# Kernel optimization log

Hardware: AMD Instinct MI355X
Metric: run time of the kernel (lower is better)

The kernel has to match this reference:

```python
import jax, jax.numpy as jnp
from jax import lax
import numpy as np

T, B, I, H, O = 256, 128, 1024, 1024, 512
SIGMA = 0.05

def setup_inputs() -> dict:
    key = jax.random.key(0)
    ks = jax.random.split(key, 16)
    x = jax.random.normal(ks[0], (T, B, I), dtype=jnp.float32)
    r_noise = jax.random.uniform(ks[1], (T, B, I), dtype=jnp.float32) * SIGMA
    z_noise = jax.random.uniform(ks[2], (T, B, I), dtype=jnp.float32) * SIGMA
    h_noise = jax.random.uniform(ks[3], (T, B, I), dtype=jnp.float32) * SIGMA
    si = 1.0 / np.sqrt(I)
    sh = 1.0 / np.sqrt(H)
    Wxz = jax.random.normal(ks[4], (H, I), dtype=jnp.float32) * si
    Wxr = jax.random.normal(ks[5], (H, I), dtype=jnp.float32) * si
    Wxh = jax.random.normal(ks[6], (H, I), dtype=jnp.float32) * si
    Whz = jax.random.normal(ks[7], (H, H), dtype=jnp.float32) * sh
    Whr = jax.random.normal(ks[8], (H, H), dtype=jnp.float32) * sh
    Whh = jax.random.normal(ks[9], (H, H), dtype=jnp.float32) * sh  # rec_scale_factor = 1.0
    bz = jnp.zeros((H,), dtype=jnp.float32)
    br = jnp.zeros((H,), dtype=jnp.float32)
    bh = jnp.zeros((H,), dtype=jnp.float32)
    Wout = jax.random.normal(ks[10], (O, H), dtype=jnp.float32) * sh
    bout = jnp.zeros((O,), dtype=jnp.float32)
    return {"x": x, "r_noise": r_noise, "z_noise": z_noise, "h_noise": h_noise,
            "Wxz": Wxz, "Wxr": Wxr, "Wxh": Wxh, "Whz": Whz, "bz": bz,
            "Whr": Whr, "br": br, "Whh": Whh, "bh": bh, "Wout": Wout, "bout": bout}

def reference(x, r_noise, z_noise, h_noise, Wxz, Wxr, Wxh, Whz, bz, Whr, br, Whh, bh, Wout, bout):
    # x: [T, B, I]; hidden state h: [B, H]
    h0 = jnp.zeros((x.shape[1], Whh.shape[0]), dtype=x.dtype)
    def step(h, inp):
        xt, rn, zn, hn = inp
        R = jax.nn.sigmoid((xt + rn) @ Wxr.T + h @ Whr.T + br)
        Z = jax.nn.sigmoid((xt + zn) @ Wxz.T + h @ Whz.T + bz)
        H_hat = jnp.tanh((xt + hn) @ Wxh.T + (R * h) @ Whh.T + bh)
        h_new = Z * h + (1.0 - Z) * H_hat
        return h_new, h_new
    _, hidden_states = lax.scan(step, h0, (x, r_noise, z_noise, h_noise))  # [T, B, H]
    out = hidden_states @ Wout.T + bout  # [T, B, O]
    return out
```

## Files before the change

### kernel.cpp

```cpp
#include <hip/hip_runtime.h>

typedef _Float16 f16;
typedef _Float16 f16x8 __attribute__((ext_vector_type(8)));
typedef _Float16 f16x4 __attribute__((ext_vector_type(4)));
typedef float    f32x4 __attribute__((ext_vector_type(4)));

#define T_STEPS 256
#define B_ROWS  128
#define I_DIM   1024
#define H_DIM   1024
#define O_DIM   512
#define TBROWS  (T_STEPS * B_ROWS)
#define BH      (B_ROWS * H_DIM)
#define NWG     64

__global__ void k_init(unsigned* flg) {
    for (int i = threadIdx.x; i < (8 * NWG + 8) * 16; i += 256) flg[i] = 0u;
}

template<int K>
__device__ __forceinline__ f16x8 gload(const f16* p) {
    f16x8 r;
    asm volatile("global_load_dwordx4 %0, %1, off offset:%c2"
                 : "=v"(r) : "v"(p), "n"(K * 64));
    return r;
}
template<int K> struct Iss {
    static __device__ __forceinline__ void go(f16x8* fr, const f16* p) {
        fr[K] = gload<K>(p);
        Iss<K + 1>::go(fr, p);
    }
};
template<> struct Iss<32> {
    static __device__ __forceinline__ void go(f16x8*, const f16*) {}
};
__device__ __forceinline__ void gstore8_cc(f16* p, f16x4 v) {
    asm volatile("global_store_dwordx2 %0, %1, off sc0 sc1"
                 :: "v"(p), "v"(v) : "memory");
}

__device__ __forceinline__ void wpub(unsigned* flg, int grp, int wg, unsigned gen, int lane) {
    asm volatile("s_waitcnt vmcnt(0) lgkmcnt(0)" ::: "memory");
    if (lane == 0)
        __hip_atomic_store(&flg[(grp * NWG + wg) * 16], gen, __ATOMIC_RELAXED, __HIP_MEMORY_SCOPE_AGENT);
    __builtin_amdgcn_sched_barrier(0);
}
__device__ __forceinline__ void wpoll(unsigned* flg, unsigned* agg, int grp, int wg, unsigned gen, int lane) {
    if (wg == grp) {
        while (__hip_atomic_load(&flg[(grp * NWG + lane) * 16], __ATOMIC_RELAXED, __HIP_MEMORY_SCOPE_AGENT) < gen)
            __builtin_amdgcn_s_sleep(1);
        if (lane < 2)
            __hip_atomic_store(&agg[grp * 16 + lane], gen, __ATOMIC_RELAXED, __HIP_MEMORY_SCOPE_AGENT);
    } else {
        while (__hip_atomic_load(&agg[grp * 16 + (lane & 1)], __ATOMIC_RELAXED, __HIP_MEMORY_SCOPE_AGENT) < gen)
            __builtin_amdgcn_s_sleep(1);
    }
    __builtin_amdgcn_sched_barrier(0);
}

__global__ __launch_bounds__(256) void k_gate_gemm(
    const float* __restrict__ x,
    const float* __restrict__ nR, const float* __restrict__ nZ, const float* __restrict__ nH,
    const float* __restrict__ WxR, const float* __restrict__ WxZ, const float* __restrict__ WxH,
    f16* __restrict__ GR, f16* __restrict__ GZ, f16* __restrict__ GH)
{
    const int g = blockIdx.z;
    const float* noise = (g == 0) ? nR : (g == 1) ? nZ : nH;
    const float* W     = (g == 0) ? WxR : (g == 1) ? WxZ : WxH;
    f16* G             = (g == 0) ? GR : (g == 1) ? GZ : GH;

    __shared__ f16 As[128 * 40];
    __shared__ f16 Bs[128 * 40];

    const int t = threadIdx.x;
    const int lane = t & 63;
    const int w  = t >> 6;
    const int wm = w & 1, wn = w >> 1;
    const int bid = blockIdx.x;
    const int l   = (bid & 7) * 256 + (bid >> 3);
    const int rowBase = (l >> 3) * 128;
    const int colBase = (l & 7) * 128;

    const int srow = t >> 1;
    const int sk   = (t & 1) * 16;

    f32x4 acc[4][4] = {};

    for (int kt = 0; kt < I_DIM; kt += 32) {
        {
            const float* xp = x     + (size_t)(rowBase + srow) * I_DIM + kt + sk;
            const float* np = noise + (size_t)(rowBase + srow) * I_DIM + kt + sk;
            f16x8 t0, t1;
            #pragma unroll
            for (int q = 0; q < 2; ++q) {
                float4 a = ((const float4*)xp)[q];
                float4 b = ((const float4*)np)[q];
                t0[q*4+0] = (f16)(a.x + b.x); t0[q*4+1] = (f16)(a.y + b.y);
                t0[q*4+2] = (f16)(a.z + b.z); t0[q*4+3] = (f16)(a.w + b.w);
            }
            #pragma unroll
            for (int q = 0; q < 2; ++q) {
                float4 a = ((const float4*)xp)[q+2];
                float4 b = ((const float4*)np)[q+2];
                t1[q*4+0] = (f16)(a.x + b.x); t1[q*4+1] = (f16)(a.y + b.y);
                t1[q*4+2] = (f16)(a.z + b.z); t1[q*4+3] = (f16)(a.w + b.w);
            }
            *(f16x8*)&As[srow*40 + sk]     = t0;
            *(f16x8*)&As[srow*40 + sk + 8] = t1;
            const float* wp = W + (size_t)(colBase + srow) * I_DIM + kt + sk;
            #pragma unroll
            for (int q = 0; q < 2; ++q) {
                float4 a = ((const float4*)wp)[q];
                t0[q*4+0] = (f16)a.x; t0[q*4+1] = (f16)a.y; t0[q*4+2] = (f16)a.z; t0[q*4+3] = (f16)a.w;
            }
            #pragma unroll
            for (int q = 0; q < 2; ++q) {
                float4 a = ((const float4*)wp)[q+2];
                t1[q*4+0] = (f16)a.x; t1[q*4+1] = (f16)a.y; t1[q*4+2] = (f16)a.z; t1[q*4+3] = (f16)a.w;
            }
            *(f16x8*)&Bs[srow*40 + sk]     = t0;
            *(f16x8*)&Bs[srow*40 + sk + 8] = t1;
        }
        __syncthreads();
        f16x8 af[4], bf[4];
        #pragma unroll
        for (int i = 0; i < 4; ++i)
            af[i] = *(const f16x8*)&As[(wm*64 + i*16 + (lane & 15))*40 + ((lane >> 4) * 8)];
        #pragma unroll
        for (int i = 0; i < 4; ++i)
            bf[i] = *(const f16x8*)&Bs[(wn*64 + i*16 + (lane & 15))*40 + ((lane >> 4) * 8)];
        #pragma unroll
        for (int i = 0; i < 4; ++i)
            #pragma unroll
            for (int j = 0; j < 4; ++j)
                acc[i][j] = __builtin_amdgcn_mfma_f32_16x16x32_f16(af[i], bf[j], acc[i][j], 0, 0, 0);
        __syncthreads();
    }
    #pragma unroll
    for (int i = 0; i < 4; ++i) {
        const int row = rowBase + wm*64 + i*16 + ((lane >> 4) * 4);
        #pragma unroll
        for (int j = 0; j < 4; ++j) {
            const int col = colBase + wn*64 + j*16 + (lane & 15);
            #pragma unroll
            for (int r = 0; r < 4; ++r)
                G[(size_t)(row + r) * H_DIM + col] = (f16)acc[i][j][r];
        }
    }
}

__global__ __launch_bounds__(256) void k_out_gemm(
    const f16* __restrict__ Hs, const float* __restrict__ Wout,
    const float* __restrict__ bout, float* __restrict__ out)
{
    __shared__ f16 As[128 * 40];
    __shared__ f16 Bs[128 * 40];

    const int t = threadIdx.x;
    const int lane = t & 63;
    const int w  = t >> 6;
    const int wm = w & 1, wn = w >> 1;
    const int bid = blockIdx.x;
    const int l   = (bid & 7) * 128 + (bid >> 3);
    const int rowBase = (l >> 2) * 128;
    const int colBase = (l & 3) * 128;

    const int srow = t >> 1;
    const int sk   = (t & 1) * 16;

    f32x4 acc[4][4] = {};

    for (int kt = 0; kt < H_DIM; kt += 32) {
        {
            const f16* ap = Hs + (size_t)(rowBase + srow) * H_DIM + kt + sk;
            *(f16x8*)&As[srow*40 + sk]     = *(const f16x8*)ap;
            *(f16x8*)&As[srow*40 + sk + 8] = *(const f16x8*)(ap + 8);
            const float* wp = Wout + (size_t)(colBase + srow) * H_DIM + kt + sk;
            f16x8 t0, t1;
            #pragma unroll
            for (int q = 0; q < 2; ++q) {
                float4 a = ((const float4*)wp)[q];
                t0[q*4+0] = (f16)a.x; t0[q*4+1] = (f16)a.y; t0[q*4+2] = (f16)a.z; t0[q*4+3] = (f16)a.w;
            }
            #pragma unroll
            for (int q = 0; q < 2; ++q) {
                float4 a = ((const float4*)wp)[q+2];
                t1[q*4+0] = (f16)a.x; t1[q*4+1] = (f16)a.y; t1[q*4+2] = (f16)a.z; t1[q*4+3] = (f16)a.w;
            }
            *(f16x8*)&Bs[srow*40 + sk]     = t0;
            *(f16x8*)&Bs[srow*40 + sk + 8] = t1;
        }
        __syncthreads();
        f16x8 af[4], bf[4];
        #pragma unroll
        for (int i = 0; i < 4; ++i)
            af[i] = *(const f16x8*)&As[(wm*64 + i*16 + (lane & 15))*40 + ((lane >> 4) * 8)];
        #pragma unroll
        for (int i = 0; i < 4; ++i)
            bf[i] = *(const f16x8*)&Bs[(wn*64 + i*16 + (lane & 15))*40 + ((lane >> 4) * 8)];
        #pragma unroll
        for (int i = 0; i < 4; ++i)
            #pragma unroll
            for (int j = 0; j < 4; ++j)
                acc[i][j] = __builtin_amdgcn_mfma_f32_16x16x32_f16(af[i], bf[j], acc[i][j], 0, 0, 0);
        __syncthreads();
    }
    #pragma unroll
    for (int i = 0; i < 4; ++i) {
        const int row = rowBase + wm*64 + i*16 + ((lane >> 4) * 4);
        #pragma unroll
        for (int j = 0; j < 4; ++j) {
            const int col = colBase + wn*64 + j*16 + (lane & 15);
            const float bb = bout[col];
            #pragma unroll
            for (int r = 0; r < 4; ++r)
                out[(size_t)(row + r) * O_DIM + col] = acc[i][j][r] + bb;
        }
    }
}

__global__ __launch_bounds__(512, 1) void k_recurrent(
    const f16* __restrict__ GR, const f16* __restrict__ GZ, const f16* __restrict__ GH,
    const float* __restrict__ WhR, const float* __restrict__ WhZ, const float* __restrict__ WhH,
    const float* __restrict__ bR, const float* __restrict__ bZ, const float* __restrict__ bH,
    f16* __restrict__ Rh_all, f16* __restrict__ Hs, unsigned* flg)
{
    __shared__ f16 WA[16 * 1032];
    __shared__ f16 WB[16 * 1032];
    __shared__ f16 WC[16 * 1032];

    unsigned* agg = flg + 8 * NWG * 16;

    const int t = threadIdx.x;
    const int lane = t & 63;
    const int w = t >> 6;
    const int wg = blockIdx.x;
    const int col0 = wg * 16;

    for (int i = t; i < 4096; i += 512) {
        int jj = i >> 8;
        int kk = (i & 255) << 2;
        float4 v = *(const float4*)(WhR + (size_t)(col0 + jj) * H_DIM + kk);
        f16x4 tv; tv[0] = (f16)v.x; tv[1] = (f16)v.y; tv[2] = (f16)v.z; tv[3] = (f16)v.w;
        *(f16x4*)&WA[jj * 1032 + kk] = tv;
        v = *(const float4*)(WhZ + (size_t)(col0 + jj) * H_DIM + kk);
        tv[0] = (f16)v.x; tv[1] = (f16)v.y; tv[2] = (f16)v.z; tv[3] = (f16)v.w;
        *(f16x4*)&WB[jj * 1032 + kk] = tv;
        v = *(const float4*)(WhH + (size_t)(col0 + jj) * H_DIM + kk);
        tv[0] = (f16)v.x; tv[1] = (f16)v.y; tv[2] = (f16)v.z; tv[3] = (f16)v.w;
        *(f16x4*)&WC[jj * 1032 + kk] = tv;
    }
    __syncthreads();

    const int brow = w * 16 + (lane & 15);
    const int arow = lane & 15;
    const int kcol = (lane >> 4) * 8;
    const int ocl  = (lane >> 4) * 4;

    const f32x4 bbr = *(const f32x4*)&bR[col0 + ocl];
    const f32x4 bbz = *(const f32x4*)&bZ[col0 + ocl];
    const f32x4 bbh = *(const f32x4*)&bH[col0 + ocl];

    const size_t eoff = (size_t)brow * H_DIM + col0 + ocl;
    const size_t koff = (size_t)brow * H_DIM + kcol;

#define CONS_RZ(B, VM)                                                           \
    asm volatile("s_waitcnt vmcnt(" #VM ")" ::: "memory");                       \
    __builtin_amdgcn_sched_barrier(0);                                           \
    _Pragma("unroll")                                                            \
    for (int i = 0; i < 8; ++i) {                                                \
        const int kk = (B) * 8 + i;                                              \
        f16x8 ar = *(const f16x8*)&WA[arow * 1032 + kk * 32 + kcol];             \
        f16x8 az = *(const f16x8*)&WB[arow * 1032 + kk * 32 + kcol];             \
        accR = __builtin_amdgcn_mfma_f32_16x16x32_f16(ar, fr[kk], accR, 0, 0, 0);\
        accZ = __builtin_amdgcn_mfma_f32_16x16x32_f16(az, fr[kk], accZ, 0, 0, 0);\
    }

#define CONS_H(B, VM)                                                            \
    asm volatile("s_waitcnt vmcnt(" #VM ")" ::: "memory");                       \
    __builtin_amdgcn_sched_barrier(0);                                           \
    _Pragma("unroll")                                                            \
    for (int i = 0; i < 8; ++i) {                                                \
        const int kk = (B) * 8 + i;                                              \
        f16x8 ah = *(const f16x8*)&WC[arow * 1032 + kk * 32 + kcol];             \
        accH = __builtin_amdgcn_mfma_f32_16x16x32_f16(ah, fr[kk], accH, 0, 0, 0);\
    }

    float h32r[4] = {0.f, 0.f, 0.f, 0.f};

    #pragma unroll 1
    for (int step = 0; step < T_STEPS; ++step) {
        const size_t sBH = (size_t)step * BH;
        f32x4 accR = {}, accZ = {};
        f16x4 gr4 = *(const f16x4*)&GR[sBH + eoff];
        f16x4 gz4 = *(const f16x4*)&GZ[sBH + eoff];
        if (step > 0) {
            wpoll(flg, agg, w, wg, 2u * (unsigned)step, lane);
            const f16* hb = Hs + (sBH - BH) + koff;
            f16x8 fr[32];
            Iss<0>::go(fr, hb);
            CONS_RZ(0, 24) CONS_RZ(1, 16) CONS_RZ(2, 8) CONS_RZ(3, 0)
        }
        float zr[4];
        f16x4 rhv;
        #pragma unroll
        for (int j = 0; j < 4; ++j) {
            float pr = accR[j] + (float)gr4[j] + bbr[j];
            float rr = 1.f / (1.f + __expf(-pr));
            rhv[j] = (f16)(rr * h32r[j]);
            float pz = accZ[j] + (float)gz4[j] + bbz[j];
            zr[j] = 1.f / (1.f + __expf(-pz));
        }
        gstore8_cc(Rh_all + sBH + eoff, rhv);
        wpub(flg, w, wg, 2u * (unsigned)step + 1u, lane);

        f32x4 accH = {};
        f16x4 gh4 = *(const f16x4*)&GH[sBH + eoff];
        wpoll(flg, agg, w, wg, 2u * (unsigned)step + 1u, lane);
        {
            const f16* rb = Rh_all + sBH + koff;
            f16x8 fr[32];
            Iss<0>::go(fr, rb);
            CONS_H(0, 24) CONS_H(1, 16) CONS_H(2, 8) CONS_H(3, 0)
        }
        f16x4 hv;
        #pragma unroll
        for (int j = 0; j < 4; ++j) {
            float ph = accH[j] + (float)gh4[j] + bbh[j];
            float e = __expf(2.f * ph);
            float th = 1.f - 2.f / (e + 1.f);
            float hn = zr[j] * h32r[j] + (1.f - zr[j]) * th;
            h32r[j] = hn;
            hv[j] = (f16)hn;
        }
        gstore8_cc(Hs + sBH + eoff, hv);
        if (step < T_STEPS - 1) wpub(flg, w, wg, 2u * (unsigned)step + 2u, lane);
    }
    asm volatile("s_waitcnt vmcnt(0)" ::: "memory");
#undef CONS_RZ
#undef CONS_H
}

extern "C" void kernel_launch(void* const* d_in, const int* in_sizes, int n_in,
                              void* d_out, int out_size, void* d_ws, size_t ws_size,
                              hipStream_t stream) {
    const float* x    = (const float*)d_in[0];
    const float* rn   = (const float*)d_in[1];
    const float* zn   = (const float*)d_in[2];
    const float* hn   = (const float*)d_in[3];
    const float* Wxz  = (const float*)d_in[4];
    const float* Wxr  = (const float*)d_in[5];
    const float* Wxh  = (const float*)d_in[6];
    const float* Whz  = (const float*)d_in[7];
    const float* bz   = (const float*)d_in[8];
    const float* Whr  = (const float*)d_in[9];
    const float* br   = (const float*)d_in[10];
    const float* Whh  = (const float*)d_in[11];
    const float* bh   = (const float*)d_in[12];
    const float* Wout = (const float*)d_in[13];
    const float* bout = (const float*)d_in[14];
    float* out = (float*)d_out;

    char* ws = (char*)d_ws;
    size_t off = 0;
    f16* GR     = (f16*)(ws + off); off += (size_t)TBROWS * H_DIM * 2;
    f16* GZ     = (f16*)(ws + off); off += (size_t)TBROWS * H_DIM * 2;
    f16* GH     = (f16*)(ws + off); off += (size_t)TBROWS * H_DIM * 2;
    f16* Hs     = (f16*)(ws + off); off += (size_t)TBROWS * H_DIM * 2;
    f16* Rh_all = (f16*)(ws + off); off += (size_t)TBROWS * H_DIM * 2;
    unsigned* flg = (unsigned*)(ws + off); off += (8 * NWG + 8) * 16 * 4;

    k_init<<<1, 256, 0, stream>>>(flg);
    k_gate_gemm<<<dim3(2048, 1, 3), 256, 0, stream>>>(
        x, rn, zn, hn, Wxr, Wxz, Wxh, GR, GZ, GH);
    k_recurrent<<<NWG, 512, 0, stream>>>(
        GR, GZ, GH, Whr, Whz, Whh, br, bz, bh, Rh_all, Hs, flg);
    k_out_gemm<<<1024, 256, 0, stream>>>(Hs, Wout, bout, out);
}
```

Measured before the change: 5.339 ms.

## Fuse input-gate GEMM into recurrent kernel and overlap via per-timestep counters

Merges the input-projection GEMM and the persistent recurrent kernel into one launch. The first 64 blocks run the recurrence and the remaining blocks compute the gate projections per timestep, each bumping an atomic counter. The recurrent blocks spin on that counter before consuming a step, so the GEMM can run on idle CUs while the latency-bound recurrence proceeds. This removes the serial GEMM phase, but it relies on the persistent blocks being scheduled first. It also changes the GEMM tiles to 512 threads with a 128x128 tile, and its output stores become cache-coherent scalar stores.

Result: faster. 4.664 ms (-12.6%).

```diff
diff --git a/kernel.cpp b/kernel.cpp
--- a/kernel.cpp
+++ b/kernel.cpp
@@ -13,9 +13,10 @@
 #define TBROWS  (T_STEPS * B_ROWS)
 #define BH      (B_ROWS * H_DIM)
 #define NWG     64
+#define GBLK    (T_STEPS * 24)
 
 __global__ void k_init(unsigned* flg) {
-    for (int i = threadIdx.x; i < (8 * NWG + 8) * 16; i += 256) flg[i] = 0u;
+    for (int i = threadIdx.x; i < (8 * NWG + 8 + 257) * 16; i += 256) flg[i] = 0u;
 }
 
 template<int K>
@@ -37,6 +38,12 @@
 __device__ __forceinline__ void gstore8_cc(f16* p, f16x4 v) {
     asm volatile("global_store_dwordx2 %0, %1, off sc0 sc1"
                  :: "v"(p), "v"(v) : "memory");
+}
+__device__ __forceinline__ void gstore2_cc(f16* p, f16 v) {
+    union { f16 f; unsigned short s; } u; u.f = v;
+    unsigned uv = u.s;
+    asm volatile("global_store_short %0, %1, off sc0 sc1"
+                 :: "v"(p), "v"(uv) : "memory");
 }
 
 __device__ __forceinline__ void wpub(unsigned* flg, int grp, int wg, unsigned gen, int lane) {
@@ -58,183 +65,106 @@
     __builtin_amdgcn_sched_barrier(0);
 }
 
-__global__ __launch_bounds__(256) void k_gate_gemm(
+__global__ __launch_bounds__(512, 1) void k_fused(
     const float* __restrict__ x,
     const float* __restrict__ nR, const float* __restrict__ nZ, const float* __restrict__ nH,
     const float* __restrict__ WxR, const float* __restrict__ WxZ, const float* __restrict__ WxH,
-    f16* __restrict__ GR, f16* __restrict__ GZ, f16* __restrict__ GH)
-{
-    const int g = blockIdx.z;
-    const float* noise = (g == 0) ? nR : (g == 1) ? nZ : nH;
-    const float* W     = (g == 0) ? WxR : (g == 1) ? WxZ : WxH;
-    f16* G             = (g == 0) ? GR : (g == 1) ? GZ : GH;
-
-    __shared__ f16 As[128 * 40];
-    __shared__ f16 Bs[128 * 40];
-
-    const int t = threadIdx.x;
-    const int lane = t & 63;
-    const int w  = t >> 6;
-    const int wm = w & 1, wn = w >> 1;
-    const int bid = blockIdx.x;
-    const int l   = (bid & 7) * 256 + (bid >> 3);
-    const int rowBase = (l >> 3) * 128;
-    const int colBase = (l & 7) * 128;
-
-    const int srow = t >> 1;
-    const int sk   = (t & 1) * 16;
-
-    f32x4 acc[4][4] = {};
-
-    for (int kt = 0; kt < I_DIM; kt += 32) {
-        {
-            const float* xp = x     + (size_t)(rowBase + srow) * I_DIM + kt + sk;
-            const float* np = noise + (size_t)(rowBase + srow) * I_DIM + kt + sk;
-            f16x8 t0, t1;
-            #pragma unroll
-            for (int q = 0; q < 2; ++q) {
-                float4 a = ((const float4*)xp)[q];
-                float4 b = ((const float4*)np)[q];
-                t0[q*4+0] = (f16)(a.x + b.x); t0[q*4+1] = (f16)(a.y + b.y);
-                t0[q*4+2] = (f16)(a.z + b.z); t0[q*4+3] = (f16)(a.w + b.w);
-            }
-            #pragma unroll
-            for (int q = 0; q < 2; ++q) {
-                float4 a = ((const float4*)xp)[q+2];
-                float4 b = ((const float4*)np)[q+2];
-                t1[q*4+0] = (f16)(a.x + b.x); t1[q*4+1] = (f16)(a.y + b.y);
-                t1[q*4+2] = (f16)(a.z + b.z); t1[q*4+3] = (f16)(a.w + b.w);
-            }
-            *(f16x8*)&As[srow*40 + sk]     = t0;
-            *(f16x8*)&As[srow*40 + sk + 8] = t1;
-            const float* wp = W + (size_t)(colBase + srow) * I_DIM + kt + sk;
-            #pragma unroll
-            for (int q = 0; q < 2; ++q) {
-                float4 a = ((const float4*)wp)[q];
-                t0[q*4+0] = (f16)a.x; t0[q*4+1] = (f16)a.y; t0[q*4+2] = (f16)a.z; t0[q*4+3] = (f16)a.w;
-            }
-            #pragma unroll
-            for (int q = 0; q < 2; ++q) {
-                float4 a = ((const float4*)wp)[q+2];
-                t1[q*4+0] = (f16)a.x; t1[q*4+1] = (f16)a.y; t1[q*4+2] = (f16)a.z; t1[q*4+3] = (f16)a.w;
-            }
-            *(f16x8*)&Bs[srow*40 + sk]     = t0;
-            *(f16x8*)&Bs[srow*40 + sk + 8] = t1;
-        }
-        __syncthreads();
-        f16x8 af[4], bf[4];
-        #pragma unroll
-        for (int i = 0; i < 4; ++i)
-            af[i] = *(const f16x8*)&As[(wm*64 + i*16 + (lane & 15))*40 + ((lane >> 4) * 8)];
-        #pragma unroll
-        for (int i = 0; i < 4; ++i)
-            bf[i] = *(const f16x8*)&Bs[(wn*64 + i*16 + (lane & 15))*40 + ((lane >> 4) * 8)];
-        #pragma unroll
-        for (int i = 0; i < 4; ++i)
-            #pragma unroll
-            for (int j = 0; j < 4; ++j)
-                acc[i][j] = __builtin_amdgcn_mfma_f32_16x16x32_f16(af[i], bf[j], acc[i][j], 0, 0, 0);
-        __syncthreads();
-    }
-    #pragma unroll
-    for (int i = 0; i < 4; ++i) {
-        const int row = rowBase + wm*64 + i*16 + ((lane >> 4) * 4);
-        #pragma unroll
-        for (int j = 0; j < 4; ++j) {
-            const int col = colBase + wn*64 + j*16 + (lane & 15);
-            #pragma unroll
-            for (int r = 0; r < 4; ++r)
-                G[(size_t)(row + r) * H_DIM + col] = (f16)acc[i][j][r];
-        }
-    }
-}
-
-__global__ __launch_bounds__(256) void k_out_gemm(
-    const f16* __restrict__ Hs, const float* __restrict__ Wout,
-    const float* __restrict__ bout, float* __restrict__ out)
-{
-    __shared__ f16 As[128 * 40];
-    __shared__ f16 Bs[128 * 40];
-
-    const int t = threadIdx.x;
-    const int lane = t & 63;
-    const int w  = t >> 6;
-    const int wm = w & 1, wn = w >> 1;
-    const int bid = blockIdx.x;
-    const int l   = (bid & 7) * 128 + (bid >> 3);
-    const int rowBase = (l >> 2) * 128;
-    const int colBase = (l & 3) * 128;
-
-    const int srow = t >> 1;
-    const int sk   = (t & 1) * 16;
-
-    f32x4 acc[4][4] = {};
-
-    for (int kt = 0; kt < H_DIM; kt += 32) {
-        {
-            const f16* ap = Hs + (size_t)(rowBase + srow) * H_DIM + kt + sk;
-            *(f16x8*)&As[srow*40 + sk]     = *(const f16x8*)ap;
-            *(f16x8*)&As[srow*40 + sk + 8] = *(const f16x8*)(ap + 8);
-            const float* wp = Wout + (size_t)(colBase + srow) * H_DIM + kt + sk;
-            f16x8 t0, t1;
-            #pragma unroll
-            for (int q = 0; q < 2; ++q) {
-                float4 a = ((const float4*)wp)[q];
-                t0[q*4+0] = (f16)a.x; t0[q*4+1] = (f16)a.y; t0[q*4+2] = (f16)a.z; t0[q*4+3] = (f16)a.w;
-            }
-            #pragma unroll
-            for (int q = 0; q < 2; ++q) {
-                float4 a = ((const float4*)wp)[q+2];
-                t1[q*4+0] = (f16)a.x; t1[q*4+1] = (f16)a.y; t1[q*4+2] = (f16)a.z; t1[q*4+3] = (f16)a.w;
-            }
-            *(f16x8*)&Bs[srow*40 + sk]     = t0;
-            *(f16x8*)&Bs[srow*40 + sk + 8] = t1;
-        }
-        __syncthreads();
-        f16x8 af[4], bf[4];
-        #pragma unroll
-        for (int i = 0; i < 4; ++i)
-            af[i] = *(const f16x8*)&As[(wm*64 + i*16 + (lane & 15))*40 + ((lane >> 4) * 8)];
-        #pragma unroll
-        for (int i = 0; i < 4; ++i)
-            bf[i] = *(const f16x8*)&Bs[(wn*64 + i*16 + (lane & 15))*40 + ((lane >> 4) * 8)];
-        #pragma unroll
-        for (int i = 0; i < 4; ++i)
-            #pragma unroll
-            for (int j = 0; j < 4; ++j)
-                acc[i][j] = __builtin_amdgcn_mfma_f32_16x16x32_f16(af[i], bf[j], acc[i][j], 0, 0, 0);
-        __syncthreads();
-    }
-    #pragma unroll
-    for (int i = 0; i < 4; ++i) {
-        const int row = rowBase + wm*64 + i*16 + ((lane >> 4) * 4);
-        #pragma unroll
-        for (int j = 0; j < 4; ++j) {
-            const int col = colBase + wn*64 + j*16 + (lane & 15);
-            const float bb = bout[col];
-            #pragma unroll
-            for (int r = 0; r < 4; ++r)
-                out[(size_t)(row + r) * O_DIM + col] = acc[i][j][r] + bb;
-        }
-    }
-}
-
-__global__ __launch_bounds__(512, 1) void k_recurrent(
-    const f16* __restrict__ GR, const f16* __restrict__ GZ, const f16* __restrict__ GH,
     const float* __restrict__ WhR, const float* __restrict__ WhZ, const float* __restrict__ WhH,
     const float* __restrict__ bR, const float* __restrict__ bZ, const float* __restrict__ bH,
+    f16* __restrict__ GR, f16* __restrict__ GZ, f16* __restrict__ GH,
     f16* __restrict__ Rh_all, f16* __restrict__ Hs, unsigned* flg)
 {
-    __shared__ f16 WA[16 * 1032];
-    __shared__ f16 WB[16 * 1032];
-    __shared__ f16 WC[16 * 1032];
+    __shared__ __align__(16) char smem[99072];
 
     unsigned* agg = flg + 8 * NWG * 16;
-
-    const int t = threadIdx.x;
+    unsigned* cnt = flg + (8 * NWG + 8) * 16;
+
+    const int bid  = blockIdx.x;
+    const int t    = threadIdx.x;
     const int lane = t & 63;
-    const int w = t >> 6;
-    const int wg = blockIdx.x;
+    const int w    = t >> 6;
+
+    if (bid >= NWG) {
+        const int gid  = bid - NWG;
+        const int s    = gid / 24;
+        const int rem  = gid - s * 24;
+        const int g    = rem >> 3;
+        const int colT = rem & 7;
+        const float* noise = (g == 0) ? nR : (g == 1) ? nZ : nH;
+        const float* W     = (g == 0) ? WxR : (g == 1) ? WxZ : WxH;
+        f16* G             = (g == 0) ? GR : (g == 1) ? GZ : GH;
+        const int rowBase = s * 128;
+        const int colBase = colT * 128;
+
+        f16* As = (f16*)smem;
+        f16* Bs = As + 128 * 40;
+
+        const int srow = t >> 2;
+        const int sk   = (t & 3) * 8;
+        const int wm = w & 1, wn = w >> 1;
+
+        f32x4 acc[4][2] = {};
+
+        for (int kt = 0; kt < I_DIM; kt += 32) {
+            {
+                const float* xp = x     + (size_t)(rowBase + srow) * I_DIM + kt + sk;
+                const float* np = noise + (size_t)(rowBase + srow) * I_DIM + kt + sk;
+                f16x8 t0;
+                #pragma unroll
+                for (int q = 0; q < 2; ++q) {
+                    float4 a = ((const float4*)xp)[q];
+                    float4 b = ((const float4*)np)[q];
+                    t0[q*4+0] = (f16)(a.x + b.x); t0[q*4+1] = (f16)(a.y + b.y);
+                    t0[q*4+2] = (f16)(a.z + b.z); t0[q*4+3] = (f16)(a.w + b.w);
+                }
+                *(f16x8*)&As[srow * 40 + sk] = t0;
+                const float* wp = W + (size_t)(colBase + srow) * I_DIM + kt + sk;
+                #pragma unroll
+                for (int q = 0; q < 2; ++q) {
+                    float4 a = ((const float4*)wp)[q];
+                    t0[q*4+0] = (f16)a.x; t0[q*4+1] = (f16)a.y;
+                    t0[q*4+2] = (f16)a.z; t0[q*4+3] = (f16)a.w;
+                }
+                *(f16x8*)&Bs[srow * 40 + sk] = t0;
+            }
+            __syncthreads();
+            f16x8 af[4], bf[2];
+            #pragma unroll
+            for (int i = 0; i < 4; ++i)
+                af[i] = *(const f16x8*)&As[(wm*64 + i*16 + (lane & 15))*40 + ((lane >> 4) * 8)];
+            #pragma unroll
+            for (int j = 0; j < 2; ++j)
+                bf[j] = *(const f16x8*)&Bs[(wn*32 + j*16 + (lane & 15))*40 + ((lane >> 4) * 8)];
+            #pragma unroll
+            for (int i = 0; i < 4; ++i)
+                #pragma unroll
+                for (int j = 0; j < 2; ++j)
+                    acc[i][j] = __builtin_amdgcn_mfma_f32_16x16x32_f16(af[i], bf[j], acc[i][j], 0, 0, 0);
+            __syncthreads();
+        }
+        #pragma unroll
+        for (int i = 0; i < 4; ++i) {
+            const int row = rowBase + wm*64 + i*16 + ((lane >> 4) * 4);
+            #pragma unroll
+            for (int j = 0; j < 2; ++j) {
+                const int col = colBase + wn*32 + j*16 + (lane & 15);
+                #pragma unroll
+                for (int r = 0; r < 4; ++r)
+                    gstore2_cc(&G[(size_t)(row + r) * H_DIM + col], (f16)acc[i][j][r]);
+            }
+        }
+        asm volatile("s_waitcnt vmcnt(0)" ::: "memory");
+        __syncthreads();
+        if (t == 0)
+            __hip_atomic_fetch_add(&cnt[s * 16], 1u, __ATOMIC_RELAXED, __HIP_MEMORY_SCOPE_AGENT);
+        return;
+    }
+
+    f16* WA = (f16*)smem;
+    f16* WB = WA + 16 * 1032;
+    f16* WC = WB + 16 * 1032;
+
+    const int wg = bid;
     const int col0 = wg * 16;
 
     for (int i = t; i < 4096; i += 512) {
@@ -287,10 +217,17 @@
     }
 
     float h32r[4] = {0.f, 0.f, 0.f, 0.f};
+    unsigned cr_next = 0;
 
     #pragma unroll 1
     for (int step = 0; step < T_STEPS; ++step) {
         const size_t sBH = (size_t)step * BH;
+        if (cr_next < 24u) {
+            while (__hip_atomic_load(&cnt[step * 16], __ATOMIC_RELAXED, __HIP_MEMORY_SCOPE_AGENT) < 24u)
+                __builtin_amdgcn_s_sleep(1);
+        }
+        __builtin_amdgcn_sched_barrier(0);
+
         f32x4 accR = {}, accZ = {};
         f16x4 gr4 = *(const f16x4*)&GR[sBH + eoff];
         f16x4 gz4 = *(const f16x4*)&GZ[sBH + eoff];
@@ -316,6 +253,8 @@
 
         f32x4 accH = {};
         f16x4 gh4 = *(const f16x4*)&GH[sBH + eoff];
+        if (step + 1 < T_STEPS)
+            cr_next = __hip_atomic_load(&cnt[(step + 1) * 16], __ATOMIC_RELAXED, __HIP_MEMORY_SCOPE_AGENT);
         wpoll(flg, agg, w, wg, 2u * (unsigned)step + 1u, lane);
         {
             const f16* rb = Rh_all + sBH + koff;
@@ -339,6 +278,76 @@
     asm volatile("s_waitcnt vmcnt(0)" ::: "memory");
 #undef CONS_RZ
 #undef CONS_H
+}
+
+__global__ __launch_bounds__(256) void k_out_gemm(
+    const f16* __restrict__ Hs, const float* __restrict__ Wout,
+    const float* __restrict__ bout, float* __restrict__ out)
+{
+    __shared__ f16 As[128 * 40];
+    __shared__ f16 Bs[128 * 40];
+
+    const int t = threadIdx.x;
+    const int lane = t & 63;
+    const int w  = t >> 6;
+    const int wm = w & 1, wn = w >> 1;
+    const int bid = blockIdx.x;
+    const int l   = (bid & 7) * 128 + (bid >> 3);
+    const int rowBase = (l >> 2) * 128;
+    const int colBase = (l & 3) * 128;
+
+    const int srow = t >> 1;
+    const int sk   = (t & 1) * 16;
+
+    f32x4 acc[4][4] = {};
+
+    for (int kt = 0; kt < H_DIM; kt += 32) {
+        {
+            const f16* ap = Hs + (size_t)(rowBase + srow) * H_DIM + kt + sk;
+            *(f16x8*)&As[srow*40 + sk]     = *(const f16x8*)ap;
+            *(f16x8*)&As[srow*40 + sk + 8] = *(const f16x8*)(ap + 8);
+            const float* wp = Wout + (size_t)(colBase + srow) * H_DIM + kt + sk;
+            f16x8 t0, t1;
+            #pragma unroll
+            for (int q = 0; q < 2; ++q) {
+                float4 a = ((const float4*)wp)[q];
+                t0[q*4+0] = (f16)a.x; t0[q*4+1] = (f16)a.y; t0[q*4+2] = (f16)a.z; t0[q*4+3] = (f16)a.w;
+            }
+            #pragma unroll
+            for (int q = 0; q < 2; ++q) {
+                float4 a = ((const float4*)wp)[q+2];
+                t1[q*4+0] = (f16)a.x; t1[q*4+1] = (f16)a.y; t1[q*4+2] = (f16)a.z; t1[q*4+3] = (f16)a.w;
+            }
+            *(f16x8*)&Bs[srow*40 + sk]     = t0;
+            *(f16x8*)&Bs[srow*40 + sk + 8] = t1;
+        }
+        __syncthreads();
+        f16x8 af[4], bf[4];
+        #pragma unroll
+        for (int i = 0; i < 4; ++i)
+            af[i] = *(const f16x8*)&As[(wm*64 + i*16 + (lane & 15))*40 + ((lane >> 4) * 8)];
+        #pragma unroll
+        for (int i = 0; i < 4; ++i)
+            bf[i] = *(const f16x8*)&Bs[(wn*64 + i*16 + (lane & 15))*40 + ((lane >> 4) * 8)];
+        #pragma unroll
+        for (int i = 0; i < 4; ++i)
+            #pragma unroll
+            for (int j = 0; j < 4; ++j)
+                acc[i][j] = __builtin_amdgcn_mfma_f32_16x16x32_f16(af[i], bf[j], acc[i][j], 0, 0, 0);
+        __syncthreads();
+    }
+    #pragma unroll
+    for (int i = 0; i < 4; ++i) {
+        const int row = rowBase + wm*64 + i*16 + ((lane >> 4) * 4);
+        #pragma unroll
+        for (int j = 0; j < 4; ++j) {
+            const int col = colBase + wn*64 + j*16 + (lane & 15);
+            const float bb = bout[col];
+            #pragma unroll
+            for (int r = 0; r < 4; ++r)
+                out[(size_t)(row + r) * O_DIM + col] = acc[i][j][r] + bb;
+        }
+    }
 }
 
 extern "C" void kernel_launch(void* const* d_in, const int* in_sizes, int n_in,
@@ -368,12 +377,11 @@
     f16* GH     = (f16*)(ws + off); off += (size_t)TBROWS * H_DIM * 2;
     f16* Hs     = (f16*)(ws + off); off += (size_t)TBROWS * H_DIM * 2;
     f16* Rh_all = (f16*)(ws + off); off += (size_t)TBROWS * H_DIM * 2;
-    unsigned* flg = (unsigned*)(ws + off); off += (8 * NWG + 8) * 16 * 4;
+    unsigned* flg = (unsigned*)(ws + off); off += (8 * NWG + 8 + 257) * 16 * 4;
 
     k_init<<<1, 256, 0, stream>>>(flg);
-    k_gate_gemm<<<dim3(2048, 1, 3), 256, 0, stream>>>(
-        x, rn, zn, hn, Wxr, Wxz, Wxh, GR, GZ, GH);
-    k_recurrent<<<NWG, 512, 0, stream>>>(
-        GR, GZ, GH, Whr, Whz, Whh, br, bz, bh, Rh_all, Hs, flg);
+    k_fused<<<NWG + GBLK, 512, 0, stream>>>(
+        x, rn, zn, hn, Wxr, Wxz, Wxh, Whr, Whz, Whh, br, bz, bh,
+        GR, GZ, GH, Rh_all, Hs, flg);
     k_out_gemm<<<1024, 256, 0, stream>>>(Hs, Wout, bout, out);
 }
```
